# Optimization experiments

Hardware: AMD Instinct MI355X
Metric: run time of the kernel (lower is better)

The kernel has to match this reference:

```python
import jax, jax.numpy as jnp
import numpy as np

N = 8192      # number of tree nodes
H = 256       # lstm_hiddens
D = 300       # word_dims (in_dim)
V = 50000     # vocab (n_embed)
K = 4         # max children per node (4-ary tree)
OUT = 4       # category_num


def _make_tree():
    # Static 4-ary tree: node i's children are 4i+1..4i+4 (if < N).
    idx = np.arange(N)[:, None] * K + 1 + np.arange(K)[None, :]
    mask = (idx < N).astype(np.float32)
    idx = np.where(idx < N, idx, 0)
    return jnp.asarray(idx, dtype=jnp.int32), jnp.asarray(mask, dtype=jnp.float32)


def setup_inputs() -> dict:
    key = jax.random.key(0)
    ks = jax.random.split(key, 6)
    xs = jax.random.randint(ks[0], (N,), 0, V, dtype=jnp.int32)
    emb_table = jax.random.normal(ks[1], (V, D), jnp.float32) * 0.1
    Wx = jax.random.normal(ks[2], (4, H, D), jnp.float32) * (1.0 / np.sqrt(D))
    bx = jnp.zeros((4, H), jnp.float32)
    Wh = jax.random.normal(ks[3], (4, H, H), jnp.float32) * (1.0 / np.sqrt(H))
    bh = jnp.zeros((4, H), jnp.float32)
    Wout = jax.random.normal(ks[4], (OUT, H), jnp.float32) * (1.0 / np.sqrt(H))
    bout = jnp.zeros((OUT,), jnp.float32)
    child_idx, child_mask = _make_tree()
    return dict(xs=xs, child_idx=child_idx, child_mask=child_mask,
                emb_table=emb_table, Wx=Wx, bx=bx, Wh=Wh, bh=bh,
                Wout=Wout, bout=bout)


def reference(xs, child_idx, child_mask, emb_table, Wx, bx, Wh, bh, Wout, bout):
    # Embedding lookup (dropout is identity in eval)
    X = emb_table[xs]                                   # [N, D]
    # Precompute all x-side gate projections in one batched matmul.
    # Gate order: 0=i, 1=f, 2=o, 3=u  (matches ix/fx/ox/ux).
    gx = jnp.einsum('ghd,nd->ngh', Wx, X) + bx          # [N, 4, H]

    Wh_i, Wh_f, Wh_o, Wh_u = Wh[0], Wh[1], Wh[2], Wh[3]
    bh_i, bh_f, bh_o, bh_u = bh[0], bh[1], bh[2], bh[3]

    def step(carry, i):
        Hbuf, Cbuf = carry
        cidx = child_idx[i]                              # [K]
        m = child_mask[i][:, None]                       # [K, 1]
        Hc = Hbuf[cidx] * m                              # [K, H] masked child h
        Cc = Cbuf[cidx] * m                              # [K, H] masked child c
        hs = Hc.sum(0)                                   # child_h_sum
        g = gx[i]                                        # [4, H]
        ig = jax.nn.sigmoid(g[0] + Wh_i @ hs + bh_i)
        og = jax.nn.sigmoid(g[2] + Wh_o @ hs + bh_o)
        ug = jnp.tanh(g[3] + Wh_u @ hs + bh_u)
        f = jax.nn.sigmoid(g[1] + Hc @ Wh_f.T + bh_f)    # [K, H] per-child forget
        c = ig * ug + (f * Cc).sum(0)                    # masked children have Cc=0
        h = og * jnp.tanh(c)
        return (Hbuf.at[i].set(h), Cbuf.at[i].set(c)), None

    order = jnp.arange(N - 1, -1, -1)                    # children before parents
    init = (jnp.zeros((N, H), X.dtype), jnp.zeros((N, H), X.dtype))
    (Hbuf, _), _ = jax.lax.scan(step, init, order)

    logits = Wout @ Hbuf[0] + bout                       # root output
    return jax.nn.log_softmax(logits)
```

## Files before the change

kernel.cpp:

```cpp
#include <hip/hip_runtime.h>


#define N_NODES 8192
#define HDIM 256
#define DDIM 300
#define GXC 1024
#define LEAF_FIRST 2048
#define WH_STRIDE 65536
#define XI(k) ((k) + (((k) >> 6) << 2))

__device__ __forceinline__ float sigf(float x) { return 1.0f / (1.0f + __expf(-x)); }

__global__ __launch_bounds__(256) void gx_leaf_gemm(
    const int* __restrict__ xs, const float* __restrict__ emb,
    const float* __restrict__ Wx, const float* __restrict__ bx,
    const float* __restrict__ bh, float* __restrict__ gx,
    float* __restrict__ Hb, float* __restrict__ Cb)
{
    __shared__ __align__(16) float As[16][68];
    __shared__ __align__(16) float Bs[3][16][68];
    const int lid  = blockIdx.x;
    const int tid  = threadIdx.x;
    const int sr   = tid >> 2;
    const int sk   = (tid & 3) << 2;
    const int trow = (tid >> 4) << 2;
    const int tcol = (tid & 15) << 2;

    if (lid < 512) {
        const int xcd = lid & 7, idx = lid >> 3;
        const int n0 = (xcd * 4 + (idx & 3)) * 64;
        const int c0 = (idx >> 2) * 64;

        const long arow = (long)xs[n0 + sr] * DDIM;
        const long brow = (long)(c0 + sr) * DDIM;

        float acc[4][4] = {};
        float4 av = *(const float4*)(emb + arow + sk);
        float4 bv = *(const float4*)(Wx  + brow + sk);

        for (int k0 = 0; k0 < DDIM; k0 += 16) {
            __syncthreads();
            As[sk+0][sr] = av.x; As[sk+1][sr] = av.y; As[sk+2][sr] = av.z; As[sk+3][sr] = av.w;
            Bs[0][sk+0][sr] = bv.x; Bs[0][sk+1][sr] = bv.y; Bs[0][sk+2][sr] = bv.z; Bs[0][sk+3][sr] = bv.w;
            __syncthreads();

            const int kn = k0 + 16;
            av = make_float4(0.f,0.f,0.f,0.f); bv = av;
            if (kn + sk < DDIM) {
                av = *(const float4*)(emb + arow + kn + sk);
                bv = *(const float4*)(Wx  + brow + kn + sk);
            }

            #pragma unroll
            for (int k = 0; k < 16; k++) {
                float4 a = *(const float4*)&As[k][trow];
                float4 b = *(const float4*)&Bs[0][k][tcol];
                float aa[4] = {a.x, a.y, a.z, a.w};
                float bb[4] = {b.x, b.y, b.z, b.w};
                #pragma unroll
                for (int i = 0; i < 4; i++)
                    #pragma unroll
                    for (int j = 0; j < 4; j++)
                        acc[i][j] = fmaf(aa[i], bb[j], acc[i][j]);
            }
        }

        const int col = c0 + tcol;
        const float4 bxa = *(const float4*)(bx + col);
        #pragma unroll
        for (int i = 0; i < 4; i++) {
            float4 r;
            r.x = acc[i][0] + bxa.x; r.y = acc[i][1] + bxa.y;
            r.z = acc[i][2] + bxa.z; r.w = acc[i][3] + bxa.w;
            *(float4*)(gx + (long)(n0 + trow + i) * GXC + col) = r;
        }
    } else {
        const int l   = lid - 512;
        const int xcd = l & 7, idx = l >> 3;
        const int n0  = LEAF_FIRST + (xcd * 12 + idx % 12) * 64;
        const int c0  = (idx / 12) * 64;

        const long arow = (long)xs[n0 + sr] * DDIM;
        const long brow0 = (long)(c0 + sr) * DDIM;
        const long brow1 = (long)(512 + c0 + sr) * DDIM;
        const long brow2 = (long)(768 + c0 + sr) * DDIM;

        float acc[3][4][4] = {};
        float4 av = *(const float4*)(emb + arow + sk);
        float4 b0 = *(const float4*)(Wx + brow0 + sk);
        float4 b1 = *(const float4*)(Wx + brow1 + sk);
        float4 b2 = *(const float4*)(Wx + brow2 + sk);

        for (int k0 = 0; k0 < DDIM; k0 += 16) {
            __syncthreads();
            As[sk+0][sr] = av.x; As[sk+1][sr] = av.y; As[sk+2][sr] = av.z; As[sk+3][sr] = av.w;
            Bs[0][sk+0][sr] = b0.x; Bs[0][sk+1][sr] = b0.y; Bs[0][sk+2][sr] = b0.z; Bs[0][sk+3][sr] = b0.w;
            Bs[1][sk+0][sr] = b1.x; Bs[1][sk+1][sr] = b1.y; Bs[1][sk+2][sr] = b1.z; Bs[1][sk+3][sr] = b1.w;
            Bs[2][sk+0][sr] = b2.x; Bs[2][sk+1][sr] = b2.y; Bs[2][sk+2][sr] = b2.z; Bs[2][sk+3][sr] = b2.w;
            __syncthreads();

            const int kn = k0 + 16;
            av = make_float4(0.f,0.f,0.f,0.f); b0 = av; b1 = av; b2 = av;
            if (kn + sk < DDIM) {
                av = *(const float4*)(emb + arow + kn + sk);
                b0 = *(const float4*)(Wx + brow0 + kn + sk);
                b1 = *(const float4*)(Wx + brow1 + kn + sk);
                b2 = *(const float4*)(Wx + brow2 + kn + sk);
            }

            #pragma unroll
            for (int k = 0; k < 16; k++) {
                float4 a = *(const float4*)&As[k][trow];
                float aa[4] = {a.x, a.y, a.z, a.w};
                #pragma unroll
                for (int g = 0; g < 3; g++) {
                    float4 b = *(const float4*)&Bs[g][k][tcol];
                    float bb[4] = {b.x, b.y, b.z, b.w};
                    #pragma unroll
                    for (int i = 0; i < 4; i++)
                        #pragma unroll
                        for (int j = 0; j < 4; j++)
                            acc[g][i][j] = fmaf(aa[i], bb[j], acc[g][i][j]);
                }
            }
        }

        const int colg = c0 + tcol;
        const float4 bxi = *(const float4*)(bx + colg);
        const float4 bxo = *(const float4*)(bx + 512 + colg);
        const float4 bxu = *(const float4*)(bx + 768 + colg);
        const float4 bhi = *(const float4*)(bh + colg);
        const float4 bho = *(const float4*)(bh + 512 + colg);
        const float4 bhu = *(const float4*)(bh + 768 + colg);
        const float bxiv[4] = {bxi.x,bxi.y,bxi.z,bxi.w};
        const float bxov[4] = {bxo.x,bxo.y,bxo.z,bxo.w};
        const float bxuv[4] = {bxu.x,bxu.y,bxu.z,bxu.w};
        const float bhiv[4] = {bhi.x,bhi.y,bhi.z,bhi.w};
        const float bhov[4] = {bho.x,bho.y,bho.z,bho.w};
        const float bhuv[4] = {bhu.x,bhu.y,bhu.z,bhu.w};
        #pragma unroll
        for (int i = 0; i < 4; i++) {
            const long row = (long)(n0 + trow + i) * HDIM + colg;
            float4 hv, cv;
            float hh[4], cc[4];
            #pragma unroll
            for (int j = 0; j < 4; j++) {
                const float gi = (acc[0][i][j] + bxiv[j]) + bhiv[j];
                const float go = (acc[1][i][j] + bxov[j]) + bhov[j];
                const float gu = (acc[2][i][j] + bxuv[j]) + bhuv[j];
                const float c  = sigf(gi) * tanhf(gu);
                const float h  = sigf(go) * tanhf(c);
                cc[j] = c; hh[j] = h;
            }
            hv.x = hh[0]; hv.y = hh[1]; hv.z = hh[2]; hv.w = hh[3];
            cv.x = cc[0]; cv.y = cc[1]; cv.z = cc[2]; cv.w = cc[3];
            *(float4*)(Hb + row) = hv;
            *(float4*)(Cb + row) = cv;
        }
    }
}

__global__ __launch_bounds__(256) void level_gemm(
    int first, int M, const float* __restrict__ Hb,
    const int* __restrict__ child_idx, const float* __restrict__ child_mask,
    const float* __restrict__ Wh, float* __restrict__ D)
{
    __shared__ __align__(16) float Xs[16][68];
    __shared__ __align__(16) float Ws[16][68];
    const int tid  = threadIdx.x;
    const int sec  = blockIdx.y;
    const int c0   = blockIdx.x * 64;
    const int r0   = blockIdx.z * 64;
    const int sr   = tid >> 2;
    const int sk   = (tid & 3) << 2;
    const int trow = (tid >> 4) << 2;
    const int tcol = (tid & 15) << 2;

    const float* Wg;
    if      (sec == 0) Wg = Wh;
    else if (sec == 1) Wg = Wh + 2 * WH_STRIDE;
    else if (sec == 2) Wg = Wh + 3 * WH_STRIDE;
    else               Wg = Wh + 1 * WH_STRIDE;

    const int  nl    = c0 + sr;
    const bool valid = nl < M;
    int   ci[4];
    float cm[4] = {0.f, 0.f, 0.f, 0.f};
    if (valid) {
        const int n = first + nl;
        if (sec < 3) {
            #pragma unroll
            for (int k = 0; k < 4; k++) {
                ci[k] = child_idx[n * 4 + k];
                cm[k] = child_mask[n * 4 + k];
            }
        } else {
            ci[0] = child_idx[n * 4 + (sec - 3)];
            cm[0] = child_mask[n * 4 + (sec - 3)];
        }
    }
    const long wrow = (long)(r0 + sr) * HDIM;

    float acc[4][4] = {};
    float4 hvr[4], wvr;

    #pragma unroll
    for (int k = 0; k < 4; k++) hvr[k] = make_float4(0.f, 0.f, 0.f, 0.f);
    if (valid) {
        if (sec < 3) {
            #pragma unroll
            for (int k = 0; k < 4; k++)
                if (cm[k] != 0.f)
                    hvr[k] = *(const float4*)(Hb + ci[k] * HDIM + sk);
        } else if (cm[0] != 0.f) {
            hvr[0] = *(const float4*)(Hb + ci[0] * HDIM + sk);
        }
    }
    wvr = *(const float4*)(Wg + wrow + sk);

    for (int k0 = 0; k0 < HDIM; k0 += 16) {
        __syncthreads();
        float4 xv;
        xv.x = hvr[0].x + hvr[1].x + hvr[2].x + hvr[3].x;
        xv.y = hvr[0].y + hvr[1].y + hvr[2].y + hvr[3].y;
        xv.z = hvr[0].z + hvr[1].z + hvr[2].z + hvr[3].z;
        xv.w = hvr[0].w + hvr[1].w + hvr[2].w + hvr[3].w;
        Xs[sk+0][sr] = xv.x; Xs[sk+1][sr] = xv.y; Xs[sk+2][sr] = xv.z; Xs[sk+3][sr] = xv.w;
        Ws[sk+0][sr] = wvr.x; Ws[sk+1][sr] = wvr.y; Ws[sk+2][sr] = wvr.z; Ws[sk+3][sr] = wvr.w;
        __syncthreads();

        const int kn = k0 + 16;
        if (kn < HDIM) {
            #pragma unroll
            for (int k = 0; k < 4; k++) hvr[k] = make_float4(0.f, 0.f, 0.f, 0.f);
            if (valid) {
                if (sec < 3) {
                    #pragma unroll
                    for (int k = 0; k < 4; k++)
                        if (cm[k] != 0.f)
                            hvr[k] = *(const float4*)(Hb + ci[k] * HDIM + kn + sk);
                } else if (cm[0] != 0.f) {
                    hvr[0] = *(const float4*)(Hb + ci[0] * HDIM + kn + sk);
                }
            }
            wvr = *(const float4*)(Wg + wrow + kn + sk);
        }

        #pragma unroll
        for (int k = 0; k < 16; k++) {
            float4 a = *(const float4*)&Ws[k][trow];
            float4 b = *(const float4*)&Xs[k][tcol];
            float avv[4] = {a.x, a.y, a.z, a.w};
            float bvv[4] = {b.x, b.y, b.z, b.w};
            #pragma unroll
            for (int i = 0; i < 4; i++)
                #pragma unroll
                for (int j = 0; j < 4; j++)
                    acc[i][j] = fmaf(avv[i], bvv[j], acc[i][j]);
        }
    }

    #pragma unroll
    for (int j = 0; j < 4; j++) {
        const int col = c0 + tcol + j;
        if (col < M) {
            float4 r;
            r.x = acc[0][j]; r.y = acc[1][j]; r.z = acc[2][j]; r.w = acc[3][j];
            *(float4*)(D + ((long)(sec * M + col)) * HDIM + r0 + trow) = r;
        }
    }
}

__global__ __launch_bounds__(256) void level_pointwise(
    int first, int M, int do_out,
    const float* __restrict__ gx, const float* __restrict__ D,
    const int* __restrict__ child_idx, const float* __restrict__ child_mask,
    const float* __restrict__ bh, float* __restrict__ Hb, float* __restrict__ Cb,
    const float* __restrict__ Wout, const float* __restrict__ bout,
    float* __restrict__ out)
{
    __shared__ float hroot[HDIM];
    __shared__ float logits[4];
    const int nl = blockIdx.x;
    const int n  = first + nl;
    const int t  = threadIdx.x;
    const float di  = D[((long)(0 * M + nl)) * HDIM + t];
    const float dO  = D[((long)(1 * M + nl)) * HDIM + t];
    const float du  = D[((long)(2 * M + nl)) * HDIM + t];
    const float* g = gx + (long)n * GXC;
    const float gi  = g[t]       + bh[t]       + di;
    const float gfb = g[256 + t] + bh[256 + t];
    const float go  = g[512 + t] + bh[512 + t] + dO;
    const float gu  = g[768 + t] + bh[768 + t] + du;

    float c = sigf(gi) * tanhf(gu);
    #pragma unroll
    for (int k = 0; k < 4; k++) {
        const float m = child_mask[n * 4 + k];
        if (m != 0.f) {
            const float df = D[((long)((3 + k) * M + nl)) * HDIM + t];
            const float cc = Cb[(long)child_idx[n * 4 + k] * HDIM + t];
            c = fmaf(sigf(gfb + df), cc, c);
        }
    }
    const float h = sigf(go) * tanhf(c);
    Hb[(long)n * HDIM + t] = h;
    Cb[(long)n * HDIM + t] = c;

    if (do_out) {
        hroot[t] = h;
        __syncthreads();
        const int o    = t >> 6;
        const int lane = t & 63;
        float s = 0.f;
        for (int jj = lane; jj < HDIM; jj += 64)
            s = fmaf(Wout[o * HDIM + jj], hroot[jj], s);
        #pragma unroll
        for (int off = 32; off > 0; off >>= 1)
            s += __shfl_down(s, off, 64);
        if (lane == 0) logits[o] = s + bout[o];
        __syncthreads();
        if (t == 0) {
            float m = logits[0];
            #pragma unroll
            for (int i = 1; i < 4; i++) m = fmaxf(m, logits[i]);
            float se = 0.f;
            #pragma unroll
            for (int i = 0; i < 4; i++) se += __expf(logits[i] - m);
            const float lse = m + __logf(se);
            #pragma unroll
            for (int i = 0; i < 4; i++) out[i] = logits[i] - lse;
        }
    }
}

__global__ __launch_bounds__(256) void tail_fused(
    int first, int M,
    const float* __restrict__ gx, const int* __restrict__ child_idx,
    const float* __restrict__ child_mask, const float* __restrict__ Wh,
    const float* __restrict__ bh, float* __restrict__ Hb, float* __restrict__ Cb)
{
    __shared__ __align__(16) float Xc[4][272];
    __shared__ __align__(16) float Xh[272];
    __shared__ float Ds[7][64];

    const int t  = threadIdx.x;
    const int nl = blockIdx.x;
    const int rb = blockIdx.y;
    const int n  = first + nl;

    {
        const int ch = t >> 6;
        const int e4 = (t & 63) << 2;
        const int cidx = child_idx[n * 4 + ch];
        const float m  = child_mask[n * 4 + ch];
        float4 v = make_float4(0.f, 0.f, 0.f, 0.f);
        if (m != 0.f) v = *(const float4*)(Hb + (long)cidx * HDIM + e4);
        *(float4*)&Xc[ch][XI(e4)] = v;
    }
    __syncthreads();
    {
        const int k = t;
        Xh[XI(k)] = Xc[0][XI(k)] + Xc[1][XI(k)] + Xc[2][XI(k)] + Xc[3][XI(k)];
    }
    __syncthreads();

    const int q = t >> 2, j = t & 3;
    const int row = rb * 64 + q;
    const float* Wi = Wh + 0 * WH_STRIDE + (long)row * HDIM;
    const float* Wf = Wh + 1 * WH_STRIDE + (long)row * HDIM;
    const float* Wo = Wh + 2 * WH_STRIDE + (long)row * HDIM;
    const float* Wu = Wh + 3 * WH_STRIDE + (long)row * HDIM;

    float a[7] = {};
    #pragma unroll 4
    for (int kk = j * 64; kk < j * 64 + 64; kk += 4) {
        const float4 wi = *(const float4*)(Wi + kk);
        const float4 wo = *(const float4*)(Wo + kk);
        const float4 wu = *(const float4*)(Wu + kk);
        const float4 wf = *(const float4*)(Wf + kk);
        const float4 hs = *(const float4*)&Xh[XI(kk)];
        a[0] += wi.x*hs.x + wi.y*hs.y + wi.z*hs.z + wi.w*hs.w;
        a[1] += wo.x*hs.x + wo.y*hs.y + wo.z*hs.z + wo.w*hs.w;
        a[2] += wu.x*hs.x + wu.y*hs.y + wu.z*hs.z + wu.w*hs.w;
        #pragma unroll
        for (int ch = 0; ch < 4; ch++) {
            const float4 cv = *(const float4*)&Xc[ch][XI(kk)];
            a[3 + ch] += wf.x*cv.x + wf.y*cv.y + wf.z*cv.z + wf.w*cv.w;
        }
    }
    #pragma unroll
    for (int s = 0; s < 7; s++) {
        float v = a[s];
        v += __shfl_xor(v, 1, 64);
        v += __shfl_xor(v, 2, 64);
        if (j == 0) Ds[s][q] = v;
    }
    __syncthreads();

    if (t < 64) {
        const int r = rb * 64 + t;
        const float* g = gx + (long)n * GXC;
        const float gi  = g[r]       + bh[r]       + Ds[0][t];
        const float gfb = g[256 + r] + bh[256 + r];
        const float go  = g[512 + r] + bh[512 + r] + Ds[1][t];
        const float gu  = g[768 + r] + bh[768 + r] + Ds[2][t];
        float c = sigf(gi) * tanhf(gu);
        #pragma unroll
        for (int ch = 0; ch < 4; ch++) {
            const float m = child_mask[n * 4 + ch];
            if (m != 0.f) {
                const float cc = Cb[(long)child_idx[n * 4 + ch] * HDIM + r];
                c = fmaf(sigf(gfb + Ds[3 + ch][t]), cc, c);
            }
        }
        const float h = sigf(go) * tanhf(c);
        Hb[(long)n * HDIM + r] = h;
        Cb[(long)n * HDIM + r] = c;
    }
}

extern "C" void kernel_launch(void* const* d_in, const int* in_sizes, int n_in,
                              void* d_out, int out_size, void* d_ws, size_t ws_size,
                              hipStream_t stream)
{
    const int*   xs         = (const int*)  d_in[0];
    const int*   child_idx  = (const int*)  d_in[1];
    const float* child_mask = (const float*)d_in[2];
    const float* emb        = (const float*)d_in[3];
    const float* Wx         = (const float*)d_in[4];
    const float* bx         = (const float*)d_in[5];
    const float* Wh         = (const float*)d_in[6];
    const float* bh         = (const float*)d_in[7];
    const float* Wout       = (const float*)d_in[8];
    const float* bout       = (const float*)d_in[9];
    float* out = (float*)d_out;

    float* gxb = (float*)d_ws;
    float* Hb  = gxb + (size_t)N_NODES * GXC;
    float* Cb  = Hb  + (size_t)N_NODES * HDIM;
    float* Dbuf = gxb + (size_t)LEAF_FIRST * GXC;

    gx_leaf_gemm<<<896, 256, 0, stream>>>(xs, emb, Wx, bx, bh, gxb, Hb, Cb);

    const int pfb[3] = {1365, 341, 85};
    const int pcb[3] = { 683, 1024, 256};
    for (int p = 0; p < 3; p++) {
        const int M = pcb[p];
        dim3 grid((M + 63) / 64, 7, 4);
        level_gemm<<<grid, 256, 0, stream>>>(pfb[p], M, Hb, child_idx, child_mask,
                                             Wh, Dbuf);
        level_pointwise<<<M, 256, 0, stream>>>(pfb[p], M, 0, gxb, Dbuf, child_idx,
                                               child_mask, bh, Hb, Cb,
                                               Wout, bout, out);
    }

    const int pft[3] = {21, 5, 1};
    const int pct[3] = {64, 16, 4};
    for (int p = 0; p < 3; p++) {
        dim3 grid(pct[p], 4);
        tail_fused<<<grid, 256, 0, stream>>>(pft[p], pct[p], gxb, child_idx,
                                             child_mask, Wh, bh, Hb, Cb);
    }

    {
        dim3 grid(1, 7, 4);
        level_gemm<<<grid, 256, 0, stream>>>(0, 1, Hb, child_idx, child_mask,
                                             Wh, Dbuf);
        level_pointwise<<<1, 256, 0, stream>>>(0, 1, 1, gxb, Dbuf, child_idx,
                                               child_mask, bh, Hb, Cb,
                                               Wout, bout, out);
    }
}
```

Baseline: 299.8 us.

## Fuse level GEMM and pointwise into multi-node kernel for large tree levels

```diff
diff --git a/kernel.cpp b/kernel.cpp
--- a/kernel.cpp
+++ b/kernel.cpp
@@ -26,8 +26,9 @@
     const int trow = (tid >> 4) << 2;
     const int tcol = (tid & 15) << 2;
 
-    if (lid < 512) {
-        const int xcd = lid & 7, idx = lid >> 3;
+    if (lid >= 384) {
+        const int l = lid - 384;
+        const int xcd = l & 7, idx = l >> 3;
         const int n0 = (xcd * 4 + (idx & 3)) * 64;
         const int c0 = (idx >> 2) * 64;
 
@@ -75,7 +76,7 @@
             *(float4*)(gx + (long)(n0 + trow + i) * GXC + col) = r;
         }
     } else {
-        const int l   = lid - 512;
+        const int l   = lid;
         const int xcd = l & 7, idx = l >> 3;
         const int n0  = LEAF_FIRST + (xcd * 12 + idx % 12) * 64;
         const int c0  = (idx / 12) * 64;
@@ -141,7 +142,6 @@
         #pragma unroll
         for (int i = 0; i < 4; i++) {
             const long row = (long)(n0 + trow + i) * HDIM + colg;
-            float4 hv, cv;
             float hh[4], cc[4];
             #pragma unroll
             for (int j = 0; j < 4; j++) {
@@ -152,11 +152,204 @@
                 const float h  = sigf(go) * tanhf(c);
                 cc[j] = c; hh[j] = h;
             }
+            float4 hv, cv;
             hv.x = hh[0]; hv.y = hh[1]; hv.z = hh[2]; hv.w = hh[3];
             cv.x = cc[0]; cv.y = cc[1]; cv.z = cc[2]; cv.w = cc[3];
             *(float4*)(Hb + row) = hv;
             *(float4*)(Cb + row) = cv;
         }
+    }
+}
+
+template<int NG>
+__global__ __launch_bounds__(256) void level_fusedN(
+    int first, int M,
+    const float* __restrict__ gx, const int* __restrict__ child_idx,
+    const float* __restrict__ child_mask, const float* __restrict__ Wh,
+    const float* __restrict__ bh, float* __restrict__ Hb, float* __restrict__ Cb)
+{
+    __shared__ __align__(16) float Xc[NG][4][272];
+    __shared__ __align__(16) float Xh[NG][272];
+    __shared__ float Ds[NG][7][64];
+
+    const int t   = threadIdx.x;
+    const int ng0 = blockIdx.x * NG;
+    const int rb  = blockIdx.y;
+
+    {
+        const int ch = t >> 6;
+        const int e4 = (t & 63) << 2;
+        #pragma unroll
+        for (int g = 0; g < NG; g++) {
+            const int nl = ng0 + g;
+            float4 v = make_float4(0.f, 0.f, 0.f, 0.f);
+            if (nl < M) {
+                const int n = first + nl;
+                const int cidx = child_idx[n * 4 + ch];
+                const float m  = child_mask[n * 4 + ch];
+                if (m != 0.f) v = *(const float4*)(Hb + (long)cidx * HDIM + e4);
+            }
+            *(float4*)&Xc[g][ch][XI(e4)] = v;
+        }
+    }
+    __syncthreads();
+    #pragma unroll
+    for (int g = 0; g < NG; g++)
+        Xh[g][XI(t)] = Xc[g][0][XI(t)] + Xc[g][1][XI(t)]
+                     + Xc[g][2][XI(t)] + Xc[g][3][XI(t)];
+    __syncthreads();
+
+    const int q = t >> 2, j = t & 3;
+    const int row = rb * 64 + q;
+    const float* Wi = Wh + 0 * WH_STRIDE + (long)row * HDIM;
+    const float* Wf = Wh + 1 * WH_STRIDE + (long)row * HDIM;
+    const float* Wo = Wh + 2 * WH_STRIDE + (long)row * HDIM;
+    const float* Wu = Wh + 3 * WH_STRIDE + (long)row * HDIM;
+
+    float a[NG][7];
+    #pragma unroll
+    for (int g = 0; g < NG; g++)
+        #pragma unroll
+        for (int s = 0; s < 7; s++) a[g][s] = 0.f;
+
+    #pragma unroll 4
+    for (int kk = j * 64; kk < j * 64 + 64; kk += 4) {
+        const float4 wi = *(const float4*)(Wi + kk);
+        const float4 wo = *(const float4*)(Wo + kk);
+        const float4 wu = *(const float4*)(Wu + kk);
+        const float4 wf = *(const float4*)(Wf + kk);
+        #pragma unroll
+        for (int g = 0; g < NG; g++) {
+            const float4 hs = *(const float4*)&Xh[g][XI(kk)];
+            a[g][0] += wi.x*hs.x + wi.y*hs.y + wi.z*hs.z + wi.w*hs.w;
+            a[g][1] += wo.x*hs.x + wo.y*hs.y + wo.z*hs.z + wo.w*hs.w;
+            a[g][2] += wu.x*hs.x + wu.y*hs.y + wu.z*hs.z + wu.w*hs.w;
+            #pragma unroll
+            for (int ch = 0; ch < 4; ch++) {
+                const float4 cv = *(const float4*)&Xc[g][ch][XI(kk)];
+                a[g][3 + ch] += wf.x*cv.x + wf.y*cv.y + wf.z*cv.z + wf.w*cv.w;
+            }
+        }
+    }
+    #pragma unroll
+    for (int g = 0; g < NG; g++)
+        #pragma unroll
+        for (int s = 0; s < 7; s++) {
+            float v = a[g][s];
+            v += __shfl_xor(v, 1, 64);
+            v += __shfl_xor(v, 2, 64);
+            if (j == 0) Ds[g][s][q] = v;
+        }
+    __syncthreads();
+
+    if (t < NG * 64) {
+        const int g   = t >> 6;
+        const int r64 = t & 63;
+        const int nl  = ng0 + g;
+        if (nl < M) {
+            const int n = first + nl;
+            const int r = rb * 64 + r64;
+            const float* gg = gx + (long)n * GXC;
+            const float gi  = gg[r]       + bh[r]       + Ds[g][0][r64];
+            const float gfb = gg[256 + r] + bh[256 + r];
+            const float go  = gg[512 + r] + bh[512 + r] + Ds[g][1][r64];
+            const float gu  = gg[768 + r] + bh[768 + r] + Ds[g][2][r64];
+            float c = sigf(gi) * tanhf(gu);
+            #pragma unroll
+            for (int ch = 0; ch < 4; ch++) {
+                const float m = child_mask[n * 4 + ch];
+                if (m != 0.f) {
+                    const float cc = Cb[(long)child_idx[n * 4 + ch] * HDIM + r];
+                    c = fmaf(sigf(gfb + Ds[g][3 + ch][r64]), cc, c);
+                }
+            }
+            const float h = sigf(go) * tanhf(c);
+            Hb[(long)n * HDIM + r] = h;
+            Cb[(long)n * HDIM + r] = c;
+        }
+    }
+}
+
+__global__ __launch_bounds__(256) void tail_fused(
+    int first, int M,
+    const float* __restrict__ gx, const int* __restrict__ child_idx,
+    const float* __restrict__ child_mask, const float* __restrict__ Wh,
+    const float* __restrict__ bh, float* __restrict__ Hb, float* __restrict__ Cb)
+{
+    __shared__ __align__(16) float Xc[4][272];
+    __shared__ __align__(16) float Xh[272];
+    __shared__ float Ds[7][64];
+
+    const int t  = threadIdx.x;
+    const int nl = blockIdx.x;
+    const int rb = blockIdx.y;
+    const int n  = first + nl;
+
+    {
+        const int ch = t >> 6;
+        const int e4 = (t & 63) << 2;
+        const int cidx = child_idx[n * 4 + ch];
+        const float m  = child_mask[n * 4 + ch];
+        float4 v = make_float4(0.f, 0.f, 0.f, 0.f);
+        if (m != 0.f) v = *(const float4*)(Hb + (long)cidx * HDIM + e4);
+        *(float4*)&Xc[ch][XI(e4)] = v;
+    }
+    __syncthreads();
+    Xh[XI(t)] = Xc[0][XI(t)] + Xc[1][XI(t)] + Xc[2][XI(t)] + Xc[3][XI(t)];
+    __syncthreads();
+
+    const int q = t >> 2, j = t & 3;
+    const int row = rb * 64 + q;
+    const float* Wi = Wh + 0 * WH_STRIDE + (long)row * HDIM;
+    const float* Wf = Wh + 1 * WH_STRIDE + (long)row * HDIM;
+    const float* Wo = Wh + 2 * WH_STRIDE + (long)row * HDIM;
+    const float* Wu = Wh + 3 * WH_STRIDE + (long)row * HDIM;
+
+    float a[7] = {};
+    #pragma unroll 4
+    for (int kk = j * 64; kk < j * 64 + 64; kk += 4) {
+        const float4 wi = *(const float4*)(Wi + kk);
+        const float4 wo = *(const float4*)(Wo + kk);
+        const float4 wu = *(const float4*)(Wu + kk);
+        const float4 wf = *(const float4*)(Wf + kk);
+        const float4 hs = *(const float4*)&Xh[XI(kk)];
+        a[0] += wi.x*hs.x + wi.y*hs.y + wi.z*hs.z + wi.w*hs.w;
+        a[1] += wo.x*hs.x + wo.y*hs.y + wo.z*hs.z + wo.w*hs.w;
+        a[2] += wu.x*hs.x + wu.y*hs.y + wu.z*hs.z + wu.w*hs.w;
+        #pragma unroll
+        for (int ch = 0; ch < 4; ch++) {
+            const float4 cv = *(const float4*)&Xc[ch][XI(kk)];
+            a[3 + ch] += wf.x*cv.x + wf.y*cv.y + wf.z*cv.z + wf.w*cv.w;
+        }
+    }
+    #pragma unroll
+    for (int s = 0; s < 7; s++) {
+        float v = a[s];
+        v += __shfl_xor(v, 1, 64);
+        v += __shfl_xor(v, 2, 64);
+        if (j == 0) Ds[s][q] = v;
+    }
+    __syncthreads();
+
+    if (t < 64) {
+        const int r = rb * 64 + t;
+        const float* g = gx + (long)n * GXC;
+        const float gi  = g[r]       + bh[r]       + Ds[0][t];
+        const float gfb = g[256 + r] + bh[256 + r];
+        const float go  = g[512 + r] + bh[512 + r] + Ds[1][t];
+        const float gu  = g[768 + r] + bh[768 + r] + Ds[2][t];
+        float c = sigf(gi) * tanhf(gu);
+        #pragma unroll
+        for (int ch = 0; ch < 4; ch++) {
+            const float m = child_mask[n * 4 + ch];
+            if (m != 0.f) {
+                const float cc = Cb[(long)child_idx[n * 4 + ch] * HDIM + r];
+                c = fmaf(sigf(gfb + Ds[3 + ch][t]), cc, c);
+            }
+        }
+        const float h = sigf(go) * tanhf(c);
+        Hb[(long)n * HDIM + r] = h;
+        Cb[(long)n * HDIM + r] = c;
     }
 }
 
@@ -334,92 +527,6 @@
     }
 }
 
-__global__ __launch_bounds__(256) void tail_fused(
-    int first, int M,
-    const float* __restrict__ gx, const int* __restrict__ child_idx,
-    const float* __restrict__ child_mask, const float* __restrict__ Wh,
-    const float* __restrict__ bh, float* __restrict__ Hb, float* __restrict__ Cb)
-{
-    __shared__ __align__(16) float Xc[4][272];
-    __shared__ __align__(16) float Xh[272];
-    __shared__ float Ds[7][64];
-
-    const int t  = threadIdx.x;
-    const int nl = blockIdx.x;
-    const int rb = blockIdx.y;
-    const int n  = first + nl;
-
-    {
-        const int ch = t >> 6;
-        const int e4 = (t & 63) << 2;
-        const int cidx = child_idx[n * 4 + ch];
-        const float m  = child_mask[n * 4 + ch];
-        float4 v = make_float4(0.f, 0.f, 0.f, 0.f);
-        if (m != 0.f) v = *(const float4*)(Hb + (long)cidx * HDIM + e4);
-        *(float4*)&Xc[ch][XI(e4)] = v;
-    }
-    __syncthreads();
-    {
-        const int k = t;
-        Xh[XI(k)] = Xc[0][XI(k)] + Xc[1][XI(k)] + Xc[2][XI(k)] + Xc[3][XI(k)];
-    }
-    __syncthreads();
-
-    const int q = t >> 2, j = t & 3;
-    const int row = rb * 64 + q;
-    const float* Wi = Wh + 0 * WH_STRIDE + (long)row * HDIM;
-    const float* Wf = Wh + 1 * WH_STRIDE + (long)row * HDIM;
-    const float* Wo = Wh + 2 * WH_STRIDE + (long)row * HDIM;
-    const float* Wu = Wh + 3 * WH_STRIDE + (long)row * HDIM;
-
-    float a[7] = {};
-    #pragma unroll 4
-    for (int kk = j * 64; kk < j * 64 + 64; kk += 4) {
-        const float4 wi = *(const float4*)(Wi + kk);
-        const float4 wo = *(const float4*)(Wo + kk);
-        const float4 wu = *(const float4*)(Wu + kk);
-        const float4 wf = *(const float4*)(Wf + kk);
-        const float4 hs = *(const float4*)&Xh[XI(kk)];
-        a[0] += wi.x*hs.x + wi.y*hs.y + wi.z*hs.z + wi.w*hs.w;
-        a[1] += wo.x*hs.x + wo.y*hs.y + wo.z*hs.z + wo.w*hs.w;
-        a[2] += wu.x*hs.x + wu.y*hs.y + wu.z*hs.z + wu.w*hs.w;
-        #pragma unroll
-        for (int ch = 0; ch < 4; ch++) {
-            const float4 cv = *(const float4*)&Xc[ch][XI(kk)];
-            a[3 + ch] += wf.x*cv.x + wf.y*cv.y + wf.z*cv.z + wf.w*cv.w;
-        }
-    }
-    #pragma unroll
-    for (int s = 0; s < 7; s++) {
-        float v = a[s];
-        v += __shfl_xor(v, 1, 64);
-        v += __shfl_xor(v, 2, 64);
-        if (j == 0) Ds[s][q] = v;
-    }
-    __syncthreads();
-
-    if (t < 64) {
-        const int r = rb * 64 + t;
-        const float* g = gx + (long)n * GXC;
-        const float gi  = g[r]       + bh[r]       + Ds[0][t];
-        const float gfb = g[256 + r] + bh[256 + r];
-        const float go  = g[512 + r] + bh[512 + r] + Ds[1][t];
-        const float gu  = g[768 + r] + bh[768 + r] + Ds[2][t];
-        float c = sigf(gi) * tanhf(gu);
-        #pragma unroll
-        for (int ch = 0; ch < 4; ch++) {
-            const float m = child_mask[n * 4 + ch];
-            if (m != 0.f) {
-                const float cc = Cb[(long)child_idx[n * 4 + ch] * HDIM + r];
-                c = fmaf(sigf(gfb + Ds[3 + ch][t]), cc, c);
-            }
-        }
-        const float h = sigf(go) * tanhf(c);
-        Hb[(long)n * HDIM + r] = h;
-        Cb[(long)n * HDIM + r] = c;
-    }
-}
-
 extern "C" void kernel_launch(void* const* d_in, const int* in_sizes, int n_in,
                               void* d_out, int out_size, void* d_ws, size_t ws_size,
                               hipStream_t stream)
@@ -443,17 +550,12 @@
 
     gx_leaf_gemm<<<896, 256, 0, stream>>>(xs, emb, Wx, bx, bh, gxb, Hb, Cb);
 
-    const int pfb[3] = {1365, 341, 85};
-    const int pcb[3] = { 683, 1024, 256};
-    for (int p = 0; p < 3; p++) {
-        const int M = pcb[p];
-        dim3 grid((M + 63) / 64, 7, 4);
-        level_gemm<<<grid, 256, 0, stream>>>(pfb[p], M, Hb, child_idx, child_mask,
-                                             Wh, Dbuf);
-        level_pointwise<<<M, 256, 0, stream>>>(pfb[p], M, 0, gxb, Dbuf, child_idx,
-                                               child_mask, bh, Hb, Cb,
-                                               Wout, bout, out);
-    }
+    level_fusedN<4><<<dim3(171, 4), 256, 0, stream>>>(1365, 683, gxb, child_idx,
+                                                      child_mask, Wh, bh, Hb, Cb);
+    level_fusedN<4><<<dim3(256, 4), 256, 0, stream>>>(341, 1024, gxb, child_idx,
+                                                      child_mask, Wh, bh, Hb, Cb);
+    level_fusedN<2><<<dim3(128, 4), 256, 0, stream>>>(85, 256, gxb, child_idx,
+                                                      child_mask, Wh, bh, Hb, Cb);
 
     const int pft[3] = {21, 5, 1};
     const int pct[3] = {64, 16, 4};
```

Result: slower. 336.9 us (+12.4%).
